# Performance work log

Measured on AMD Instinct MI355X. Metric: run time of the kernel, lower is better.

## Reference

```python
import jax, jax.numpy as jnp
from jax import lax
import numpy as np

B, E, K, CAP = 512, 16, 2, 64
H = W = 32
ALPHA, LOAD_PEN, MIN_USE, RTEMP = 0.7, 2.0, 0.05, 1.0


def _conv(x, w, b):
    y = lax.conv_general_dilated(x, w, (1, 1), 'SAME', dimension_numbers=('NCHW', 'OIHW', 'NCHW'))
    return y + b[None, :, None, None]


def _bn(x, s, b):
    # eval-mode BatchNorm2d: running_mean=0, running_var=1 folded into scale/bias
    return x * s[None, :, None, None] + b[None, :, None, None]


def _ln(x, g, b, eps=1e-5):
    m = x.mean(-1, keepdims=True)
    v = ((x - m) ** 2).mean(-1, keepdims=True)
    return (x - m) * lax.rsqrt(v + eps) * g + b


def _maxpool(x):
    return lax.reduce_window(x, -jnp.inf, lax.max, (1, 1, 2, 2), (1, 1, 2, 2), 'VALID')


def setup_inputs() -> dict:
    key = jax.random.key(0)
    ks = iter(jax.random.split(key, 64))

    def nrm(shape, fan_in):
        return jax.random.normal(next(ks), shape, jnp.float32) / float(np.sqrt(fan_in))

    inp = {'x': jax.random.normal(next(ks), (B, 3, H, W), jnp.float32)}
    for i, (ci, co) in enumerate([(3, 64), (64, 64), (64, 128), (128, 128), (128, 256), (256, 256)], 1):
        inp[f'conv_w{i}'] = nrm((co, ci, 3, 3), ci * 9)
        inp[f'conv_b{i}'] = jnp.zeros((co,), jnp.float32)
        inp[f'bn_s{i}'] = jnp.ones((co,), jnp.float32)
        inp[f'bn_b{i}'] = jnp.zeros((co,), jnp.float32)
    inp['gate_w1'] = nrm((E, 64, 256), 256); inp['gate_b1'] = jnp.zeros((E, 64)); inp['gate_g1'] = jnp.ones((E, 64)); inp['gate_bb1'] = jnp.zeros((E, 64))
    inp['gate_w2'] = nrm((E, 32, 64), 64); inp['gate_b2'] = jnp.zeros((E, 32))
    inp['gate_w3'] = nrm((E, 1, 32), 32); inp['gate_b3'] = jnp.zeros((E, 1))
    inp['exp_w1'] = nrm((E, 256, 256), 256); inp['exp_b1'] = jnp.zeros((E, 256)); inp['exp_g1'] = jnp.ones((E, 256)); inp['exp_bb1'] = jnp.zeros((E, 256))
    inp['exp_w2'] = nrm((E, 128, 256), 256); inp['exp_b2'] = jnp.zeros((E, 128)); inp['exp_g2'] = jnp.ones((E, 128)); inp['exp_bb2'] = jnp.zeros((E, 128))
    inp['exp_w3'] = nrm((E, 128, 128), 128); inp['exp_b3'] = jnp.zeros((E, 128))
    inp['cls_w'] = nrm((E, 10, 128), 128); inp['cls_b'] = jnp.zeros((E, 10))
    return inp


def _forward(x, conv_w1, conv_b1, bn_s1, bn_b1, conv_w2, conv_b2, bn_s2, bn_b2,
             conv_w3, conv_b3, bn_s3, bn_b3, conv_w4, conv_b4, bn_s4, bn_b4,
             conv_w5, conv_b5, bn_s5, bn_b5, conv_w6, conv_b6, bn_s6, bn_b6,
             gate_w1, gate_b1, gate_g1, gate_bb1, gate_w2, gate_b2, gate_w3, gate_b3,
             exp_w1, exp_b1, exp_g1, exp_bb1, exp_w2, exp_b2, exp_g2, exp_bb2,
             exp_w3, exp_b3, cls_w, cls_b):
    # ---- trunk (eval: dropout = identity) ----
    h = jax.nn.relu(_bn(_conv(x, conv_w1, conv_b1), bn_s1, bn_b1))
    h = jax.nn.relu(_bn(_conv(h, conv_w2, conv_b2), bn_s2, bn_b2))
    h = _maxpool(h)
    h = jax.nn.relu(_bn(_conv(h, conv_w3, conv_b3), bn_s3, bn_b3))
    h = jax.nn.relu(_bn(_conv(h, conv_w4, conv_b4), bn_s4, bn_b4))
    h = _maxpool(h)
    h = jax.nn.relu(_bn(_conv(h, conv_w5, conv_b5), bn_s5, bn_b5))
    h = jax.nn.relu(_bn(_conv(h, conv_w6, conv_b6), bn_s6, bn_b6))
    feats = h.mean((2, 3))  # AdaptiveAvgPool2d(1) + Flatten -> [B, 256]
    # ---- experts (vectorized over E) ----
    h1 = jax.nn.relu(_ln(jnp.einsum('bc,eoc->beo', feats, exp_w1) + exp_b1, exp_g1, exp_bb1))
    h2 = jax.nn.relu(_ln(jnp.einsum('beh,eoh->beo', h1, exp_w2) + exp_b2, exp_g2, exp_bb2))
    embeds = jnp.einsum('beh,eoh->beo', h2, exp_w3) + exp_b3  # [B, E, 128]
    logits_e = jnp.einsum('bed,ecd->bec', embeds, cls_w) + cls_b  # [B, E, 10]
    probs = jax.nn.softmax(logits_e, axis=2)
    entropy = -(probs * jnp.log(probs + 1e-12)).sum(-1)  # [B, E]
    confidence = -entropy
    # ---- gates (vectorized over E) ----
    g1 = jax.nn.relu(_ln(jnp.einsum('bc,eoc->beo', feats, gate_w1) + gate_b1, gate_g1, gate_bb1))
    g2 = jax.nn.relu(jnp.einsum('beh,eoh->beo', g1, gate_w2) + gate_b2)
    scores = (jnp.einsum('beh,eoh->beo', g2, gate_w3) + gate_b3)[..., 0] / RTEMP  # [B, E]
    # ---- top-k capacity routing (eval: usage_ema at init = 1/E, no noise) ----
    usage = jnp.full((E,), 1.0 / E, jnp.float32)
    combined = ALPHA * scores + (1.0 - ALPHA) * confidence
    combined = combined + jnp.where(usage < MIN_USE, (MIN_USE - usage) * 10.0, 0.0)[None, :]
    balanced = combined - LOAD_PEN * usage[None, :]
    _, topk_idx = lax.top_k(balanced, K)  # [B, K]

    def step(loads, idx_row):
        lt = loads[idx_row]  # [K]
        avail = lt < CAP
        chosen = jnp.where(jnp.any(avail), idx_row[jnp.argmax(avail)], idx_row[jnp.argmin(lt)])
        return loads.at[chosen].add(1.0), chosen

    _, chosen = lax.scan(step, jnp.zeros((E,), jnp.float32), topk_idx)
    D = jax.nn.one_hot(chosen, E, dtype=jnp.bool_)  # [B, E]
    masked = jnp.where(D, balanced, -jnp.inf)
    rw = jax.nn.softmax(masked, axis=1) * D
    rw = rw / (rw.sum(1, keepdims=True) + 1e-12)
    final_logits = jnp.einsum('be,bec->bc', rw, logits_e)
    return final_logits, balanced, D


def reference(x, conv_w1, conv_b1, bn_s1, bn_b1, conv_w2, conv_b2, bn_s2, bn_b2,
              conv_w3, conv_b3, bn_s3, bn_b3, conv_w4, conv_b4, bn_s4, bn_b4,
              conv_w5, conv_b5, bn_s5, bn_b5, conv_w6, conv_b6, bn_s6, bn_b6,
              gate_w1, gate_b1, gate_g1, gate_bb1, gate_w2, gate_b2, gate_w3, gate_b3,
              exp_w1, exp_b1, exp_g1, exp_bb1, exp_w2, exp_b2, exp_g2, exp_bb2,
              exp_w3, exp_b3, cls_w, cls_b):
    return _forward(x, conv_w1, conv_b1, bn_s1, bn_b1, conv_w2, conv_b2, bn_s2, bn_b2,
                    conv_w3, conv_b3, bn_s3, bn_b3, conv_w4, conv_b4, bn_s4, bn_b4,
                    conv_w5, conv_b5, bn_s5, bn_b5, conv_w6, conv_b6, bn_s6, bn_b6,
                    gate_w1, gate_b1, gate_g1, gate_bb1, gate_w2, gate_b2, gate_w3, gate_b3,
                    exp_w1, exp_b1, exp_g1, exp_bb1, exp_w2, exp_b2, exp_g2, exp_bb2,
                    exp_w3, exp_b3, cls_w, cls_b)
```

## Files before the change

kernel.cpp:

```cpp
#include <hip/hip_runtime.h>


typedef _Float16 h16;
typedef _Float16 half8 __attribute__((ext_vector_type(8)));
typedef float f32x16 __attribute__((ext_vector_type(16)));

__device__ __forceinline__ void split2f(float x, h16& hh, h16& ll) {
  h16 a = (h16)x;
  hh = a;
  ll = (h16)(x - (float)a);
}

__device__ __forceinline__ void dma_b16(const h16* g, h16* l) {
  __builtin_amdgcn_global_load_lds(
      (const __attribute__((address_space(1))) void*)g,
      (__attribute__((address_space(3))) void*)l, 16, 0, 0);
}

__global__ void prep_all_k(const float* __restrict__ cw1, const float* __restrict__ cw2,
                           const float* __restrict__ cw3, const float* __restrict__ cw4,
                           const float* __restrict__ cw5, const float* __restrict__ cw6,
                           float* __restrict__ wt1t, h16* __restrict__ wh,
                           h16* p0, h16* p1, h16* p2, h16* p3) {
  int idx = blockIdx.x * 256 + threadIdx.x;
  if (idx < 64) {
    h16* p = (idx < 16) ? p0 : (idx < 32) ? p1 : (idx < 48) ? p2 : p3;
    p[idx & 15] = (h16)0.f;
    return;
  }
  idx -= 64;
  if (idx < 1728) {
    int co = idx % 64, r = idx / 64;
    wt1t[idx] = cw1[(size_t)co * 27 + r];
    return;
  }
  idx -= 1728;
  const float* w; int CIN, COUT; size_t off;
  if (idx < 36864)        { w = cw2; CIN = 64;  COUT = 64;  off = 0; }
  else if (idx < 110592)  { w = cw3; CIN = 64;  COUT = 128; off = 36864;  idx -= 36864; }
  else if (idx < 258048)  { w = cw4; CIN = 128; COUT = 128; off = 110592; idx -= 110592; }
  else if (idx < 552960)  { w = cw5; CIN = 128; COUT = 256; off = 258048; idx -= 258048; }
  else if (idx < 1142784) { w = cw6; CIN = 256; COUT = 256; off = 552960; idx -= 552960; }
  else return;
  int KCOB = COUT >> 6;
  int lidx = idx;
  int c8   = idx & 7;
  int t    = idx >> 3;
  int co64 = t & 63;  t >>= 6;
  int half = t & 1;   t >>= 1;
  int cob  = t % KCOB; t /= KCOB;
  int tap  = t % 9;
  int ck   = t / 9;
  int ci = ck * 16 + half * 8 + c8;
  int co = cob * 64 + co64;
  float v = w[((size_t)co * CIN + ci) * 9 + tap];
  wh[off + lidx] = (h16)v;
}

__global__ __launch_bounds__(256) void conv1_k(
    const float* __restrict__ x, const float* __restrict__ wt,
    const float* __restrict__ cb, const float* __restrict__ bns,
    const float* __restrict__ bnb, h16* __restrict__ oh, h16* __restrict__ ol)
{
  __shared__ float sx[3 * 34 * 34];
  const int tid = threadIdx.x;
  const int img = blockIdx.x;
  for (int idx = tid; idx < 3 * 34 * 34; idx += 256) {
    int xx = idx % 34;
    int t  = idx / 34;
    int rr = t % 34;
    int c  = t / 34;
    int gr = rr - 1, gx = xx - 1;
    float v = 0.f;
    if (gr >= 0 && gr < 32 && gx >= 0 && gx < 32)
      v = x[((size_t)(img * 3 + c) * 32 + gr) * 32 + gx];
    sx[(c * 34 + rr) * 34 + xx] = v;
  }
  __syncthreads();
#pragma unroll 1
  for (int k = 0; k < 4; ++k) {
    int px = k * 256 + tid;
    int yy = px >> 5, xx = px & 31;
    float in27[27];
#pragma unroll
    for (int c = 0; c < 3; ++c)
#pragma unroll
      for (int dy = 0; dy < 3; ++dy)
#pragma unroll
        for (int dx = 0; dx < 3; ++dx)
          in27[c * 9 + dy * 3 + dx] = sx[(c * 34 + yy + dy) * 34 + xx + dx];
#pragma unroll 1
    for (int cbk = 0; cbk < 4; ++cbk) {
      h16 hb[16], lb[16];
#pragma unroll
      for (int j = 0; j < 16; ++j) {
        int co = cbk * 16 + j;
        float acc = 0.f;
#pragma unroll
        for (int t = 0; t < 27; ++t) acc = fmaf(in27[t], wt[t * 64 + co], acc);
        float s = bns[co];
        float yv = fmaxf(fmaf(acc + cb[co], s, bnb[co]), 0.f);
        split2f(yv, hb[j], lb[j]);
      }
      size_t o = 16 + ((size_t)(img * 4 + cbk) * 1024 + px) * 16;
      *(half8*)&oh[o]     = *(half8*)&hb[0];
      *(half8*)&oh[o + 8] = *(half8*)&hb[8];
      *(half8*)&ol[o]     = *(half8*)&lb[0];
      *(half8*)&ol[o + 8] = *(half8*)&lb[8];
    }
  }
}

template<int H, int W, int CIN, int COUT, int MT, int POOL, int OCC>
__global__ __launch_bounds__(256, OCC) void conv_mfma(
    const h16* __restrict__ Ah, const h16* __restrict__ Al,
    const h16* __restrict__ Wh,
    const float* __restrict__ cb, const float* __restrict__ bns,
    const float* __restrict__ bnb,
    h16* __restrict__ Oh, h16* __restrict__ Ol, float* __restrict__ feats)
{
  constexpr int TPI  = (H * W) / 32;
  constexpr int RPT  = 32 / W;
  constexpr int IPB  = (4 * MT * 32 >= H * W) ? (4 * MT * 32) / (H * W) : 1;
  constexpr int KC   = CIN / 16;
  constexpr int HW   = H * W;
  constexpr int KCO  = COUT / 16;
  constexpr int KCOB = COUT / 64;
  constexpr int LOGW = (W == 32) ? 5 : (W == 16) ? 4 : 3;
  constexpr int PF   = (MT == 1) ? 3 : 2;

  __shared__ h16 sBh[2][9 * 2 * 64 * 8];
  __shared__ float sRed[(POOL == 2 && MT == 1) ? 256 : 1];

  const int tid  = threadIdx.x;
  const int lane = tid & 63;
  const int wave = tid >> 6;
  const int half = lane >> 5;
  const int col  = lane & 31;
  const int cob  = blockIdx.z;
  const int co0  = cob * 64;

  int aoff[MT], ty[MT], tx[MT], img_t[MT], rw0[MT];
#pragma unroll
  for (int t = 0; t < MT; ++t) {
    int gt   = blockIdx.y * (4 * MT) + wave * MT + t;
    int img  = blockIdx.x * IPB + gt / TPI;
    int row0 = (gt % TPI) * RPT;
    int y = row0 + (col >> LOGW);
    int x = col & (W - 1);
    img_t[t] = img; rw0[t] = row0; ty[t] = y; tx[t] = x;
    aoff[t] = 16 + ((img * KC) * HW + y * W + x) * 16 + half * 8;
  }

  f32x16 acc[MT][2];
#pragma unroll
  for (int t = 0; t < MT; ++t)
#pragma unroll
    for (int n = 0; n < 2; ++n)
#pragma unroll
      for (int i = 0; i < 16; ++i) acc[t][n][i] = 0.f;

#pragma unroll
  for (int i = 0; i < 5; ++i) {
    int id = tid + i * 256;
    if (id < 1152) {
      int src = ((id >> 7) * KCOB + cob) * 1024 + (id & 127) * 8;
      dma_b16(Wh + src, &sBh[0][id * 8]);
    }
  }
  __syncthreads();

  int buf = 0;
#pragma unroll 1
  for (int ck = 0; ck < KC; ++ck) {
    const bool have_next = (ck + 1 < KC);
    if (have_next) {
#pragma unroll
      for (int i = 0; i < 5; ++i) {
        int id = tid + i * 256;
        if (id < 1152) {
          int src = (((ck + 1) * 9 + (id >> 7)) * KCOB + cob) * 1024 + (id & 127) * 8;
          dma_b16(Wh + src, &sBh[buf ^ 1][id * 8]);
        }
      }
    }

    const int ckoA = ck * (HW * 16);
    const h16* bB = sBh[buf];

    half8 pah[PF][MT], pal[PF][MT];
#pragma unroll
    for (int pt = 0; pt < PF; ++pt) {
      const int dy = pt / 3 - 1, dx = pt % 3 - 1;
      const int ashift = (dy * W + dx) * 16;
#pragma unroll
      for (int t = 0; t < MT; ++t) {
        bool v = ((unsigned)(ty[t] + dy) < (unsigned)H) &&
                 ((unsigned)(tx[t] + dx) < (unsigned)W);
        int ai = v ? (aoff[t] + ckoA + ashift) : (half * 8);
        pah[pt][t] = *(const half8*)(Ah + ai);
        pal[pt][t] = *(const half8*)(Al + ai);
      }
    }

#pragma unroll
    for (int tap = 0; tap < 9; ++tap) {
      const int bufr = tap % PF;
      half8 bh[2];
#pragma unroll
      for (int n = 0; n < 2; ++n) {
        int bi = ((tap * 2 + half) * 64 + n * 32 + col) * 8;
        bh[n] = *(const half8*)&bB[bi];
      }
      half8 cah[MT], cal[MT];
#pragma unroll
      for (int t = 0; t < MT; ++t) { cah[t] = pah[bufr][t]; cal[t] = pal[bufr][t]; }
      if (tap + PF < 9) {
        const int pt = tap + PF;
        const int dy = pt / 3 - 1, dx = pt % 3 - 1;
        const int ashift = (dy * W + dx) * 16;
#pragma unroll
        for (int t = 0; t < MT; ++t) {
          bool v = ((unsigned)(ty[t] + dy) < (unsigned)H) &&
                   ((unsigned)(tx[t] + dx) < (unsigned)W);
          int ai = v ? (aoff[t] + ckoA + ashift) : (half * 8);
          pah[bufr][t] = *(const half8*)(Ah + ai);
          pal[bufr][t] = *(const half8*)(Al + ai);
        }
      }
#pragma unroll
      for (int t = 0; t < MT; ++t)
#pragma unroll
        for (int n = 0; n < 2; ++n) {
          acc[t][n] = __builtin_amdgcn_mfma_f32_32x32x16_f16(cah[t], bh[n], acc[t][n], 0, 0, 0);
          acc[t][n] = __builtin_amdgcn_mfma_f32_32x32x16_f16(cal[t], bh[n], acc[t][n], 0, 0, 0);
        }
    }

    __syncthreads();
    buf ^= 1;
  }

#pragma unroll
  for (int n = 0; n < 2; ++n) {
    const int co = co0 + n * 32 + col;
    const float es = bns[co];
    const float eb = fmaf(cb[co], es, bnb[co]);
    const int cko = co >> 4, c16 = co & 15;

    if constexpr (POOL == 0) {
#pragma unroll
      for (int t = 0; t < MT; ++t) {
#pragma unroll
        for (int r = 0; r < 16; ++r) {
          float v = fmaxf(fmaf(acc[t][n][r], es, eb), 0.f);
          int m = (r & 3) + 4 * half + 8 * (r >> 2);
          int y = rw0[t] + (m >> LOGW);
          int x = m & (W - 1);
          size_t oi = 16 + ((size_t)(img_t[t] * KCO + cko) * HW + y * W + x) * 16 + c16;
          h16 hh, ll; split2f(v, hh, ll);
          Oh[oi] = hh; Ol[oi] = ll;
        }
      }
    } else if constexpr (POOL == 1 && RPT == 1) {
      constexpr int HWq = (H / 2) * (W / 2);
#pragma unroll
      for (int tp = 0; tp < MT / 2; ++tp) {
        const int t0 = 2 * tp, t1 = 2 * tp + 1;
        const int yq = rw0[t0] >> 1;
#pragma unroll
        for (int r = 0; r < 16; r += 2) {
          float v00 = fmaxf(fmaf(acc[t0][n][r],     es, eb), 0.f);
          float v01 = fmaxf(fmaf(acc[t0][n][r + 1], es, eb), 0.f);
          float v10 = fmaxf(fmaf(acc[t1][n][r],     es, eb), 0.f);
          float v11 = fmaxf(fmaf(acc[t1][n][r + 1], es, eb), 0.f);
          float mv = fmaxf(fmaxf(v00, v01), fmaxf(v10, v11));
          int xq = ((r & 3) >> 1) + 2 * half + 4 * (r >> 2);
          size_t oi = 16 + ((size_t)(img_t[t0] * KCO + cko) * HWq + yq * (W / 2) + xq) * 16 + c16;
          h16 hh, ll; split2f(mv, hh, ll);
          Oh[oi] = hh; Ol[oi] = ll;
        }
      }
    } else if constexpr (POOL == 1) {
      constexpr int HWq = (H / 2) * (W / 2);
#pragma unroll
      for (int t = 0; t < MT; ++t) {
        const int yq = rw0[t] >> 1;
#pragma unroll
        for (int r = 0; r < 8; r += 2) {
          float v00 = fmaxf(fmaf(acc[t][n][r],     es, eb), 0.f);
          float v01 = fmaxf(fmaf(acc[t][n][r + 1], es, eb), 0.f);
          float v10 = fmaxf(fmaf(acc[t][n][r + 8], es, eb), 0.f);
          float v11 = fmaxf(fmaf(acc[t][n][r + 9], es, eb), 0.f);
          float mv = fmaxf(fmaxf(v00, v01), fmaxf(v10, v11));
          int xq = ((r & 3) >> 1) + 2 * half + 4 * (r >> 2);
          size_t oi = 16 + ((size_t)(img_t[t] * KCO + cko) * HWq + yq * (W / 2) + xq) * 16 + c16;
          h16 hh, ll; split2f(mv, hh, ll);
          Oh[oi] = hh; Ol[oi] = ll;
        }
      }
    } else if constexpr (POOL == 2 && MT == 1) {
      float s = 0.f;
#pragma unroll
      for (int r = 0; r < 16; ++r)
        s += fmaxf(fmaf(acc[0][n][r], es, eb), 0.f);
      s += __shfl_xor(s, 32, 64);
      if (half == 0) sRed[wave * 64 + n * 32 + col] = s;
    } else if constexpr (POOL == 2) {
      float s = 0.f;
#pragma unroll
      for (int t = 0; t < MT; ++t)
#pragma unroll
        for (int r = 0; r < 16; ++r)
          s += fmaxf(fmaf(acc[t][n][r], es, eb), 0.f);
      s += __shfl_xor(s, 32, 64);
      if (half == 0) feats[(size_t)img_t[0] * 256 + co] = s * (1.f / 64.f);
    }
  }

  if constexpr (POOL == 2 && MT == 1) {
    __syncthreads();
    if (tid < 128) {
      int li = tid >> 6, co_l = tid & 63;
      float s = sRed[(li * 2) * 64 + co_l] + sRed[(li * 2 + 1) * 64 + co_l];
      feats[(size_t)(blockIdx.x * 2 + li) * 256 + co0 + co_l] = s * (1.f / 64.f);
    }
  }
}

template<int O, int K, int LN, int RELU>
__global__ __launch_bounds__(256, 4) void gemm_head(
    const float* __restrict__ A, size_t aStrideE,
    const float* __restrict__ Wm, const float* __restrict__ bias,
    const float* __restrict__ g, const float* __restrict__ bb,
    float* __restrict__ out)
{
  constexpr int KC  = (O >= 256) ? 32 : 64;
  constexpr int WST = O + 4;
  constexpr int TO  = O / 16;
  __shared__ float sA[KC * 36];
  __shared__ float sW[KC * WST];
  __shared__ float mArr[32], rArr[32];

  const int tid  = threadIdx.x;
  const int lane = tid & 63;
  const int wave = tid >> 6;
  const int e    = blockIdx.y;
  const int b0g  = blockIdx.x * 32;
  const int bl   = (lane & 15) * 2;
  const int ol   = wave * (O / 4) + (lane >> 4) * TO;

  const float* Ae = A + (size_t)e * aStrideE;
  const float* We = Wm + (size_t)e * O * K;

  float acc[2][TO];
#pragma unroll
  for (int i = 0; i < 2; ++i)
#pragma unroll
    for (int j = 0; j < TO; ++j) acc[i][j] = 0.f;

  for (int k0 = 0; k0 < K; k0 += KC) {
    for (int idx = tid; idx < 32 * KC; idx += 256) {
      int kk = idx % KC, bb_ = idx / KC;
      sA[kk * 36 + bb_] = Ae[(size_t)(b0g + bb_) * K + k0 + kk];
    }
    for (int idx = tid; idx < O * KC; idx += 256) {
      int kk = idx % KC, oo = idx / KC;
      sW[kk * WST + oo] = We[(size_t)oo * K + k0 + kk];
    }
    __syncthreads();
#pragma unroll 4
    for (int kk = 0; kk < KC; ++kk) {
      float2 av = *(const float2*)&sA[kk * 36 + bl];
      float a2[2] = {av.x, av.y};
#pragma unroll
      for (int j4 = 0; j4 < TO; j4 += 4) {
        float4 wv = *(const float4*)&sW[kk * WST + ol + j4];
        float w4[4] = {wv.x, wv.y, wv.z, wv.w};
#pragma unroll
        for (int i = 0; i < 2; ++i)
#pragma unroll
          for (int jj = 0; jj < 4; ++jj)
            acc[i][j4 + jj] = fmaf(a2[i], w4[jj], acc[i][j4 + jj]);
      }
    }
    __syncthreads();
  }

  const float* bi = bias + (size_t)e * O;
#pragma unroll
  for (int i = 0; i < 2; ++i)
#pragma unroll
    for (int j = 0; j < TO; ++j) acc[i][j] += bi[ol + j];

  if constexpr (LN) {
    float* redS = sA;
    float* redQ = sA + 512;
    const int grp = wave * 4 + (lane >> 4);
#pragma unroll
    for (int i = 0; i < 2; ++i) {
      float s = 0.f, q = 0.f;
#pragma unroll
      for (int j = 0; j < TO; ++j) { s += acc[i][j]; q += acc[i][j] * acc[i][j]; }
      redS[(bl + i) * 16 + grp] = s;
      redQ[(bl + i) * 16 + grp] = q;
    }
    __syncthreads();
    if (tid < 32) {
      float s = 0.f, q = 0.f;
#pragma unroll
      for (int gi = 0; gi < 16; ++gi) { s += redS[tid * 16 + gi]; q += redQ[tid * 16 + gi]; }
      float mean = s * (1.f / O);
      float var  = q * (1.f / O) - mean * mean;
      mArr[tid] = mean;
      rArr[tid] = rsqrtf(var + 1e-5f);
    }
    __syncthreads();
    const float* gp  = g + (size_t)e * O;
    const float* bbp = bb + (size_t)e * O;
#pragma unroll
    for (int i = 0; i < 2; ++i) {
      float mean = mArr[bl + i], rstd = rArr[bl + i];
#pragma unroll
      for (int j = 0; j < TO; ++j)
        acc[i][j] = (acc[i][j] - mean) * rstd * gp[ol + j] + bbp[ol + j];
    }
  }
  if constexpr (RELU) {
#pragma unroll
    for (int i = 0; i < 2; ++i)
#pragma unroll
      for (int j = 0; j < TO; ++j) acc[i][j] = fmaxf(acc[i][j], 0.f);
  }
#pragma unroll
  for (int i = 0; i < 2; ++i) {
    float* op = out + ((size_t)e * 512 + b0g + bl + i) * O + ol;
#pragma unroll
    for (int j4 = 0; j4 < TO; j4 += 4)
      *(float4*)(op + j4) = make_float4(acc[i][j4], acc[i][j4 + 1], acc[i][j4 + 2], acc[i][j4 + 3]);
  }
}

__global__ void heads_small_k(const float* __restrict__ embeds,
                              const float* __restrict__ cw,
                              const float* __restrict__ cbias,
                              const float* __restrict__ g1, const float* __restrict__ w2,
                              const float* __restrict__ b2, const float* __restrict__ w3,
                              const float* __restrict__ b3,
                              float* __restrict__ logits_e, float* __restrict__ conf,
                              float* __restrict__ scores)
{
  int wv   = (blockIdx.x * 256 + threadIdx.x) >> 6;
  int lane = threadIdx.x & 63;
  int b = wv >> 4, e = wv & 15;

  const float* ep = embeds + ((size_t)e * 512 + b) * 128;
  float e0 = ep[lane], e1 = ep[lane + 64];
  float l[10];
#pragma unroll
  for (int o = 0; o < 10; ++o) {
    const float* wp = cw + ((size_t)e * 10 + o) * 128;
    l[o] = e0 * wp[lane] + e1 * wp[lane + 64];
  }
#pragma unroll
  for (int s = 32; s >= 1; s >>= 1)
#pragma unroll
    for (int o = 0; o < 10; ++o) l[o] += __shfl_xor(l[o], s, 64);
#pragma unroll
  for (int o = 0; o < 10; ++o) l[o] += cbias[e * 10 + o];
  float m = l[0];
#pragma unroll
  for (int o = 1; o < 10; ++o) m = fmaxf(m, l[o]);
  float p[10], sum = 0.f;
#pragma unroll
  for (int o = 0; o < 10; ++o) { p[o] = expf(l[o] - m); sum += p[o]; }
  float inv = 1.f / sum, ent = 0.f;
#pragma unroll
  for (int o = 0; o < 10; ++o) { float pp = p[o] * inv; ent -= pp * logf(pp + 1e-12f); }
  if (lane == 0) {
    conf[b * 16 + e] = -ent;
#pragma unroll
    for (int o = 0; o < 10; ++o) logits_e[((size_t)b * 16 + e) * 10 + o] = l[o];
  }

  float gv = g1[((size_t)e * 512 + b) * 64 + lane];
  const float* w3p = w3 + e * 32;
  float sc = 0.f;
#pragma unroll
  for (int o = 0; o < 32; ++o) {
    float t = gv * w2[((size_t)e * 32 + o) * 64 + lane];
#pragma unroll
    for (int s = 32; s >= 1; s >>= 1) t += __shfl_xor(t, s, 64);
    float g2v = fmaxf(t + b2[e * 32 + o], 0.f);
    sc = fmaf(g2v, w3p[o], sc);
  }
  if (lane == 0) scores[b * 16 + e] = sc + b3[e];
}

__global__ void routing_k(const float* __restrict__ scores, const float* __restrict__ conf,
                          const float* __restrict__ logits_e, float* __restrict__ out)
{
  __shared__ int t2[512];
  __shared__ int chs[512];
  const int tid = threadIdx.x;

  if (tid < 512) {
    int b = tid;
    float v0 = -3.4e38f, v1 = -3.4e38f;
    int i0 = 0, i1 = 0;
#pragma unroll
    for (int e = 0; e < 16; ++e) {
      float s = scores[b * 16 + e];
      float c = conf[b * 16 + e];
      float v = 0.7f * s + 0.3f * c - 0.125f;
      out[5120 + b * 16 + e] = v;
      if (v > v0) { v1 = v0; i1 = i0; v0 = v; i0 = e; }
      else if (v > v1) { v1 = v; i1 = e; }
    }
    t2[b] = i0 | (i1 << 8);
  }
  __syncthreads();

  if (tid < 64) {
    int lane = tid;
    int cnt = 0;
    int pk[8];
#pragma unroll
    for (int k = 0; k < 8; ++k) pk[k] = t2[k * 64 + lane];
#pragma unroll 1
    for (int k = 0; k < 8; ++k) {
      for (int j = 0; j < 64; ++j) {
        int pair = __shfl(pk[k], j, 64);
        int i0 = pair & 0xff, i1 = (pair >> 8) & 0xff;
        int c0 = __shfl(cnt, i0, 64);
        int c1 = __shfl(cnt, i1, 64);
        int ch = (c0 < 64) ? i0 : ((c1 < 64) ? i1 : ((c0 <= c1) ? i0 : i1));
        cnt += (lane == ch) ? 1 : 0;
        if (lane == 0) chs[k * 64 + j] = ch;
      }
    }
  }
  __syncthreads();

  if (tid < 512) {
    int b = tid;
    int ch = chs[b];
#pragma unroll
    for (int e = 0; e < 16; ++e)
      out[13312 + b * 16 + e] = (e == ch) ? 1.0f : 0.0f;
#pragma unroll
    for (int o = 0; o < 10; ++o)
      out[b * 10 + o] = logits_e[((size_t)b * 16 + ch) * 10 + o];
  }
}

extern "C" void kernel_launch(void* const* d_in, const int* in_sizes, int n_in,
                              void* d_out, int out_size, void* d_ws, size_t ws_size,
                              hipStream_t stream) {
  (void)in_sizes; (void)n_in; (void)out_size; (void)ws_size;

  const float* x = (const float*)d_in[0];
  const float *cw[6], *cbv[6], *bsv[6], *bbv[6];
  for (int i = 0; i < 6; ++i) {
    cw[i]  = (const float*)d_in[1 + 4 * i];
    cbv[i] = (const float*)d_in[2 + 4 * i];
    bsv[i] = (const float*)d_in[3 + 4 * i];
    bbv[i] = (const float*)d_in[4 + 4 * i];
  }
  const float* gate_w1  = (const float*)d_in[25];
  const float* gate_b1  = (const float*)d_in[26];
  const float* gate_g1  = (const float*)d_in[27];
  const float* gate_bb1 = (const float*)d_in[28];
  const float* gate_w2  = (const float*)d_in[29];
  const float* gate_b2  = (const float*)d_in[30];
  const float* gate_w3  = (const float*)d_in[31];
  const float* gate_b3  = (const float*)d_in[32];
  const float* exp_w1   = (const float*)d_in[33];
  const float* exp_b1   = (const float*)d_in[34];
  const float* exp_g1   = (const float*)d_in[35];
  const float* exp_bb1  = (const float*)d_in[36];
  const float* exp_w2   = (const float*)d_in[37];
  const float* exp_b2   = (const float*)d_in[38];
  const float* exp_g2   = (const float*)d_in[39];
  const float* exp_bb2  = (const float*)d_in[40];
  const float* exp_w3   = (const float*)d_in[41];
  const float* exp_b3   = (const float*)d_in[42];
  const float* cls_w    = (const float*)d_in[43];
  const float* cls_b    = (const float*)d_in[44];

  char* wsb = (char*)d_ws;
  const size_t off_wt1t = 0;
  const size_t off_whi  = 6912;
  const size_t off_Phi  = 4578048;
  const size_t off_Plo  = 71687168;
  const size_t off_Qhi  = 138796288;
  const size_t off_Qlo  = 155573760;
  const size_t off_feats= 172351232;
  const size_t off_h1   = 138796288 + 512;
  const size_t off_h2   = off_h1 + 8388608;
  const size_t off_emb  = off_h2 + 4194304;
  const size_t off_g1   = off_emb + 4194304;
  const size_t off_lg   = off_g1 + 2097152;
  const size_t off_conf = off_lg + 327680;
  const size_t off_sc   = off_conf + 32768;

  float* wt1t = (float*)(wsb + off_wt1t);
  h16* whi = (h16*)(wsb + off_whi);
  h16* Phi = (h16*)(wsb + off_Phi);
  h16* Plo = (h16*)(wsb + off_Plo);
  h16* Qhi = (h16*)(wsb + off_Qhi);
  h16* Qlo = (h16*)(wsb + off_Qlo);
  float* feats = (float*)(wsb + off_feats);
  float* h1 = (float*)(wsb + off_h1);
  float* h2 = (float*)(wsb + off_h2);
  float* emb = (float*)(wsb + off_emb);
  float* g1 = (float*)(wsb + off_g1);
  float* lg = (float*)(wsb + off_lg);
  float* conf = (float*)(wsb + off_conf);
  float* sc = (float*)(wsb + off_sc);

  const size_t wo2 = 0;
  const size_t wo3 = 36864;
  const size_t wo4 = 110592;
  const size_t wo5 = 258048;
  const size_t wo6 = 552960;

  prep_all_k<<<4471, 256, 0, stream>>>(cw[0], cw[1], cw[2], cw[3], cw[4], cw[5],
                                       wt1t, whi, Phi, Plo, Qhi, Qlo);

  conv1_k<<<512, 256, 0, stream>>>(x, wt1t, cbv[0], bsv[0], bbv[0], Phi, Plo);
  conv_mfma<32, 32, 64, 64, 2, 1, 3><<<dim3(512, 4, 1), 256, 0, stream>>>(
      Phi, Plo, whi + wo2, cbv[1], bsv[1], bbv[1], Qhi, Qlo, nullptr);
  conv_mfma<16, 16, 64, 128, 2, 0, 3><<<dim3(512, 1, 2), 256, 0, stream>>>(
      Qhi, Qlo, whi + wo3, cbv[2], bsv[2], bbv[2], Phi, Plo, nullptr);
  conv_mfma<16, 16, 128, 128, 2, 1, 3><<<dim3(512, 1, 2), 256, 0, stream>>>(
      Phi, Plo, whi + wo4, cbv[3], bsv[3], bbv[3], Qhi, Qlo, nullptr);
  conv_mfma<8, 8, 128, 256, 1, 0, 4><<<dim3(256, 1, 4), 256, 0, stream>>>(
      Qhi, Qlo, whi + wo5, cbv[4], bsv[4], bbv[4], Phi, Plo, nullptr);
  conv_mfma<8, 8, 256, 256, 1, 2, 4><<<dim3(256, 1, 4), 256, 0, stream>>>(
      Phi, Plo, whi + wo6, cbv[5], bsv[5], bbv[5], nullptr, nullptr, feats);

  gemm_head<256, 256, 1, 1><<<dim3(16, 16), 256, 0, stream>>>(
      feats, (size_t)0, exp_w1, exp_b1, exp_g1, exp_bb1, h1);
  gemm_head<64, 256, 1, 1><<<dim3(16, 16), 256, 0, stream>>>(
      feats, (size_t)0, gate_w1, gate_b1, gate_g1, gate_bb1, g1);
  gemm_head<128, 256, 1, 1><<<dim3(16, 16), 256, 0, stream>>>(
      h1, (size_t)512 * 256, exp_w2, exp_b2, exp_g2, exp_bb2, h2);
  gemm_head<128, 128, 0, 0><<<dim3(16, 16), 256, 0, stream>>>(
      h2, (size_t)512 * 128, exp_w3, exp_b3, nullptr, nullptr, emb);
  heads_small_k<<<2048, 256, 0, stream>>>(emb, cls_w, cls_b,
                                          g1, gate_w2, gate_b2, gate_w3, gate_b3,
                                          lg, conf, sc);

  routing_k<<<1, 512, 0, stream>>>(sc, conf, lg, (float*)d_out);
}
```

Before: 725.7 us.

## Stage conv activation tiles with halo in LDS instead of per-tap global loads

The MFMA conv kernel now DMAs each block's activation rows plus a one-row halo (hi and lo planes) into shared memory alongside the weights. All 9 taps then read from LDS rather than issuing repeated global loads from registers-prefetched buffers. A DBUF template flag picks double buffering for the 8x8 layers and single buffering with an extra barrier for the larger layers to limit LDS use. Occupancy hints for the 8x8 layers drop from 4 to 3, and the pool reduction scratch now reuses the activation LDS. The single-buffered path serializes loads and compute, and the larger LDS footprint may reduce occupancy.

```diff
diff --git a/kernel.cpp b/kernel.cpp
--- a/kernel.cpp
+++ b/kernel.cpp
@@ -111,7 +111,7 @@
   }
 }
 
-template<int H, int W, int CIN, int COUT, int MT, int POOL, int OCC>
+template<int H, int W, int CIN, int COUT, int MT, int POOL, int OCC, int DBUF>
 __global__ __launch_bounds__(256, OCC) void conv_mfma(
     const h16* __restrict__ Ah, const h16* __restrict__ Al,
     const h16* __restrict__ Wh,
@@ -127,10 +127,17 @@
   constexpr int KCO  = COUT / 16;
   constexpr int KCOB = COUT / 64;
   constexpr int LOGW = (W == 32) ? 5 : (W == 16) ? 4 : 3;
-  constexpr int PF   = (MT == 1) ? 3 : 2;
-
-  __shared__ h16 sBh[2][9 * 2 * 64 * 8];
-  __shared__ float sRed[(POOL == 2 && MT == 1) ? 256 : 1];
+  constexpr int ROWS_COV = (4 * MT * 32) / (W * IPB);
+  constexpr int ROFF  = (ROWS_COV < H) ? 1 : 0;
+  constexpr int SROWS = ROWS_COV + 2 * ROFF;
+  constexpr int ASZ = IPB * SROWS * W * 16;
+  constexpr int ACH = ASZ / 8;
+  constexpr int NBUF = DBUF ? 2 : 1;
+  constexpr int TCH  = 1152 + 2 * ACH;
+  constexpr int NI   = (TCH + 255) / 256;
+
+  __shared__ h16 sB[NBUF][9 * 2 * 64 * 8];
+  __shared__ h16 sA[NBUF][2][ASZ + 16];
 
   const int tid  = threadIdx.x;
   const int lane = tid & 63;
@@ -139,17 +146,46 @@
   const int col  = lane & 31;
   const int cob  = blockIdx.z;
   const int co0  = cob * 64;
-
-  int aoff[MT], ty[MT], tx[MT], img_t[MT], rw0[MT];
+  const int r0img = blockIdx.y * ROWS_COV;
+
+  auto STAGE = [&](int ck, int nb) {
+#pragma unroll
+    for (int i = 0; i < NI; ++i) {
+      int id = tid + i * 256;
+      if (id < 1152) {
+        int src = ((ck * 9 + (id >> 7)) * KCOB + cob) * 1024 + (id & 127) * 8;
+        dma_b16(Wh + src, &sB[nb][id * 8]);
+      } else if (id < TCH) {
+        int c2  = id - 1152;
+        int pl  = c2 / ACH;
+        int cc  = c2 - pl * ACH;
+        int hs  = cc & 1;
+        int pxg = cc >> 1;
+        int iL  = pxg / (SROWS * W);
+        int rem = pxg - iL * (SROWS * W);
+        int rs  = rem / W;
+        int px  = rem - rs * W;
+        int grow = r0img + rs - ROFF;
+        if (ROFF == 0 || ((unsigned)grow < (unsigned)H)) {
+          const h16* gp = pl ? Al : Ah;
+          int srcA = 16 + (((blockIdx.x * IPB + iL) * KC + ck) * HW + grow * W + px) * 16 + hs * 8;
+          dma_b16(gp + srcA, &sA[nb][pl][cc * 8]);
+        }
+      }
+    }
+  };
+
+  int sbase[MT], ty[MT], tx[MT], img_t[MT], rw0[MT];
 #pragma unroll
   for (int t = 0; t < MT; ++t) {
     int gt   = blockIdx.y * (4 * MT) + wave * MT + t;
+    int imgL = (gt / TPI) % IPB;
     int img  = blockIdx.x * IPB + gt / TPI;
     int row0 = (gt % TPI) * RPT;
     int y = row0 + (col >> LOGW);
     int x = col & (W - 1);
     img_t[t] = img; rw0[t] = row0; ty[t] = y; tx[t] = x;
-    aoff[t] = 16 + ((img * KC) * HW + y * W + x) * 16 + half * 8;
+    sbase[t] = (imgL * SROWS + (y - r0img + ROFF)) * W + x;
   }
 
   f32x16 acc[MT][2];
@@ -160,85 +196,59 @@
 #pragma unroll
       for (int i = 0; i < 16; ++i) acc[t][n][i] = 0.f;
 
-#pragma unroll
-  for (int i = 0; i < 5; ++i) {
-    int id = tid + i * 256;
-    if (id < 1152) {
-      int src = ((id >> 7) * KCOB + cob) * 1024 + (id & 127) * 8;
-      dma_b16(Wh + src, &sBh[0][id * 8]);
-    }
-  }
+  if (tid < NBUF * 2 * 16) {
+    int wsl = tid >> 4;
+    sA[wsl >> 1][wsl & 1][ASZ + (tid & 15)] = (h16)0.f;
+  }
+  STAGE(0, 0);
   __syncthreads();
 
   int buf = 0;
 #pragma unroll 1
   for (int ck = 0; ck < KC; ++ck) {
-    const bool have_next = (ck + 1 < KC);
-    if (have_next) {
-#pragma unroll
-      for (int i = 0; i < 5; ++i) {
-        int id = tid + i * 256;
-        if (id < 1152) {
-          int src = (((ck + 1) * 9 + (id >> 7)) * KCOB + cob) * 1024 + (id & 127) * 8;
-          dma_b16(Wh + src, &sBh[buf ^ 1][id * 8]);
-        }
-      }
-    }
-
-    const int ckoA = ck * (HW * 16);
-    const h16* bB = sBh[buf];
-
-    half8 pah[PF][MT], pal[PF][MT];
-#pragma unroll
-    for (int pt = 0; pt < PF; ++pt) {
-      const int dy = pt / 3 - 1, dx = pt % 3 - 1;
-      const int ashift = (dy * W + dx) * 16;
+    if constexpr (DBUF) {
+      if (ck + 1 < KC) STAGE(ck + 1, buf ^ 1);
+    }
+    const h16* bB = &sB[buf][0];
+    const h16* aH = &sA[buf][0][0];
+    const h16* aL = &sA[buf][1][0];
+    const int zoff = ASZ + half * 8;
+
+#pragma unroll
+    for (int tap = 0; tap < 9; ++tap) {
+      const int dy = tap / 3 - 1, dx = tap % 3 - 1;
+      half8 bh[2];
+#pragma unroll
+      for (int n = 0; n < 2; ++n)
+        bh[n] = *(const half8*)&bB[((tap * 2 + half) * 64 + n * 32 + col) * 8];
+      half8 ah[MT], al[MT];
 #pragma unroll
       for (int t = 0; t < MT; ++t) {
         bool v = ((unsigned)(ty[t] + dy) < (unsigned)H) &&
                  ((unsigned)(tx[t] + dx) < (unsigned)W);
-        int ai = v ? (aoff[t] + ckoA + ashift) : (half * 8);
-        pah[pt][t] = *(const half8*)(Ah + ai);
-        pal[pt][t] = *(const half8*)(Al + ai);
-      }
-    }
-
-#pragma unroll
-    for (int tap = 0; tap < 9; ++tap) {
-      const int bufr = tap % PF;
-      half8 bh[2];
-#pragma unroll
-      for (int n = 0; n < 2; ++n) {
-        int bi = ((tap * 2 + half) * 64 + n * 32 + col) * 8;
-        bh[n] = *(const half8*)&bB[bi];
-      }
-      half8 cah[MT], cal[MT];
-#pragma unroll
-      for (int t = 0; t < MT; ++t) { cah[t] = pah[bufr][t]; cal[t] = pal[bufr][t]; }
-      if (tap + PF < 9) {
-        const int pt = tap + PF;
-        const int dy = pt / 3 - 1, dx = pt % 3 - 1;
-        const int ashift = (dy * W + dx) * 16;
-#pragma unroll
-        for (int t = 0; t < MT; ++t) {
-          bool v = ((unsigned)(ty[t] + dy) < (unsigned)H) &&
-                   ((unsigned)(tx[t] + dx) < (unsigned)W);
-          int ai = v ? (aoff[t] + ckoA + ashift) : (half * 8);
-          pah[bufr][t] = *(const half8*)(Ah + ai);
-          pal[bufr][t] = *(const half8*)(Al + ai);
+        int po = v ? ((sbase[t] + dy * W + dx) * 16 + half * 8) : zoff;
+        ah[t] = *(const half8*)(aH + po);
+        al[t] = *(const half8*)(aL + po);
+      }
+#pragma unroll
+      for (int t = 0; t < MT; ++t)
+#pragma unroll
+        for (int n = 0; n < 2; ++n) {
+          acc[t][n] = __builtin_amdgcn_mfma_f32_32x32x16_f16(ah[t], bh[n], acc[t][n], 0, 0, 0);
+          acc[t][n] = __builtin_amdgcn_mfma_f32_32x32x16_f16(al[t], bh[n], acc[t][n], 0, 0, 0);
         }
-      }
-#pragma unroll
-      for (int t = 0; t < MT; ++t)
-#pragma unroll
-        for (int n = 0; n < 2; ++n) {
-          acc[t][n] = __builtin_amdgcn_mfma_f32_32x32x16_f16(cah[t], bh[n], acc[t][n], 0, 0, 0);
-          acc[t][n] = __builtin_amdgcn_mfma_f32_32x32x16_f16(cal[t], bh[n], acc[t][n], 0, 0, 0);
-        }
-    }
-
-    __syncthreads();
-    buf ^= 1;
+    }
+
+    if constexpr (DBUF) {
+      __syncthreads();
+      buf ^= 1;
+    } else {
+      __syncthreads();
+      if (ck + 1 < KC) {
+        STAGE(ck + 1, 0);
+        __syncthreads();
+      }
+    }
   }
 
 #pragma unroll
@@ -300,12 +310,13 @@
         }
       }
     } else if constexpr (POOL == 2 && MT == 1) {
+      float* sRd = (float*)&sA[0][0][0];
       float s = 0.f;
 #pragma unroll
       for (int r = 0; r < 16; ++r)
         s += fmaxf(fmaf(acc[0][n][r], es, eb), 0.f);
       s += __shfl_xor(s, 32, 64);
-      if (half == 0) sRed[wave * 64 + n * 32 + col] = s;
+      if (half == 0) sRd[wave * 64 + n * 32 + col] = s;
     } else if constexpr (POOL == 2) {
       float s = 0.f;
 #pragma unroll
@@ -319,10 +330,11 @@
   }
 
   if constexpr (POOL == 2 && MT == 1) {
+    float* sRd = (float*)&sA[0][0][0];
     __syncthreads();
     if (tid < 128) {
       int li = tid >> 6, co_l = tid & 63;
-      float s = sRed[(li * 2) * 64 + co_l] + sRed[(li * 2 + 1) * 64 + co_l];
+      float s = sRd[(li * 2) * 64 + co_l] + sRd[(li * 2 + 1) * 64 + co_l];
       feats[(size_t)(blockIdx.x * 2 + li) * 256 + co0 + co_l] = s * (1.f / 64.f);
     }
   }
@@ -629,15 +641,15 @@
                                        wt1t, whi, Phi, Plo, Qhi, Qlo);
 
   conv1_k<<<512, 256, 0, stream>>>(x, wt1t, cbv[0], bsv[0], bbv[0], Phi, Plo);
-  conv_mfma<32, 32, 64, 64, 2, 1, 3><<<dim3(512, 4, 1), 256, 0, stream>>>(
+  conv_mfma<32, 32, 64, 64, 2, 1, 3, 0><<<dim3(512, 4, 1), 256, 0, stream>>>(
       Phi, Plo, whi + wo2, cbv[1], bsv[1], bbv[1], Qhi, Qlo, nullptr);
-  conv_mfma<16, 16, 64, 128, 2, 0, 3><<<dim3(512, 1, 2), 256, 0, stream>>>(
+  conv_mfma<16, 16, 64, 128, 2, 0, 3, 0><<<dim3(512, 1, 2), 256, 0, stream>>>(
       Qhi, Qlo, whi + wo3, cbv[2], bsv[2], bbv[2], Phi, Plo, nullptr);
-  conv_mfma<16, 16, 128, 128, 2, 1, 3><<<dim3(512, 1, 2), 256, 0, stream>>>(
+  conv_mfma<16, 16, 128, 128, 2, 1, 3, 0><<<dim3(512, 1, 2), 256, 0, stream>>>(
       Phi, Plo, whi + wo4, cbv[3], bsv[3], bbv[3], Qhi, Qlo, nullptr);
-  conv_mfma<8, 8, 128, 256, 1, 0, 4><<<dim3(256, 1, 4), 256, 0, stream>>>(
+  conv_mfma<8, 8, 128, 256, 1, 0, 3, 1><<<dim3(256, 1, 4), 256, 0, stream>>>(
       Qhi, Qlo, whi + wo5, cbv[4], bsv[4], bbv[4], Phi, Plo, nullptr);
-  conv_mfma<8, 8, 256, 256, 1, 2, 4><<<dim3(256, 1, 4), 256, 0, stream>>>(
+  conv_mfma<8, 8, 256, 256, 1, 2, 3, 1><<<dim3(256, 1, 4), 256, 0, stream>>>(
       Phi, Plo, whi + wo6, cbv[5], bsv[5], bbv[5], nullptr, nullptr, feats);
 
   gemm_head<256, 256, 1, 1><<<dim3(16, 16), 256, 0, stream>>>(
```

New measurement: 722.6 us. About the same (-0.4%).
